# Optimization experiments

Hardware: AMD Instinct MI355X
Metric: run time of the kernel (lower is better)

Reference implementation:

```python
import jax, jax.numpy as jnp
import numpy as np

B, D = 4096, 768

def setup_inputs() -> dict:
    key = jax.random.key(0)
    k1, k2 = jax.random.split(key)
    embeddings = jax.random.normal(k1, (B, D), dtype=jnp.float32)
    # precomputed articulatory distance matrix (stand-in for articulatory_distance_fn over word pairs)
    art_dist = jax.random.uniform(k2, (B, B), dtype=jnp.float32)
    return {"embeddings": embeddings, "art_dist": art_dist}

def reference(embeddings, art_dist):
    b = embeddings.shape[0]
    # pairwise squared L2 distances via Gram matrix: ||ei||^2 + ||ej||^2 - 2 ei.ej
    sq = jnp.sum(embeddings * embeddings, axis=1)                  # [B]
    gram = jnp.einsum('id,jd->ij', embeddings, embeddings)         # [B, B]
    d2 = sq[:, None] + sq[None, :] - 2.0 * gram                    # [B, B]
    off_diag = 1.0 - jnp.eye(b, dtype=embeddings.dtype)            # exclude i == j
    pair_loss = (d2 - art_dist) ** 2
    pairs_count = b * (b - 1)
    return jnp.sum(pair_loss * off_diag) / pairs_count
```

## Files before the change

### kernel.cpp

```cpp
#include <hip/hip_runtime.h>
#include <hip/hip_bf16.h>

#define B_DIM 4096
#define D_DIM 768
#define BM 128
#define BN 128
#define BK 64

typedef __bf16 bf16_t;
typedef bf16_t bf16x8 __attribute__((ext_vector_type(8)));
typedef float f32x4 __attribute__((ext_vector_type(4)));

__global__ __launch_bounds__(256) void prep_kernel(
    const float* __restrict__ E, ushort* __restrict__ Ebf, float* __restrict__ sq)
{
    const int row = blockIdx.x;
    const int tid = threadIdx.x;
    const float* er = E + (size_t)row * D_DIM;
    ushort* br = Ebf + (size_t)row * D_DIM;
    float s = 0.f;
    #pragma unroll
    for (int c = tid; c < D_DIM; c += 256) {
        float v = er[c];
        s += v * v;
        __hip_bfloat16 h = __float2bfloat16(v);
        br[c] = *reinterpret_cast<const ushort*>(&h);
    }
    #pragma unroll
    for (int off = 32; off > 0; off >>= 1) s += __shfl_down(s, off);
    __shared__ float red[4];
    if ((tid & 63) == 0) red[tid >> 6] = s;
    __syncthreads();
    if (tid == 0) sq[row] = red[0] + red[1] + red[2] + red[3];
}

__global__ __launch_bounds__(256) void gram_loss_kernel(
    const ushort* __restrict__ Ebf, const float* __restrict__ sq,
    const float* __restrict__ art, float* __restrict__ out)
{
    __shared__ ushort Als[BM][BK];
    __shared__ ushort Bls[BN][BK];
    __shared__ float red[4];

    const int tid  = threadIdx.x;
    const int lane = tid & 63;
    const int wave = tid >> 6;
    const int wr = wave >> 1;
    const int wc = wave & 1;
    const int tileR = blockIdx.x >> 5;
    const int tileC = blockIdx.x & 31;
    const int row0 = tileR * BM;
    const int col0 = tileC * BN;

    f32x4 acc[4][4] = {};

    const int srow  = tid >> 3;
    const int scol8 = (tid & 7) * 8;

    for (int kk = 0; kk < D_DIM; kk += BK) {
        #pragma unroll
        for (int i = 0; i < 4; ++i) {
            const int r = i * 32 + srow;
            const int colg = scol8 ^ ((r & 7) << 3);
            const ushort* gA = Ebf + (size_t)(row0 + r) * D_DIM + kk + colg;
            __builtin_amdgcn_global_load_lds(
                (const __attribute__((address_space(1))) void*)gA,
                (__attribute__((address_space(3))) void*)(&Als[r][scol8]),
                16, 0, 0);
            const ushort* gB = Ebf + (size_t)(col0 + r) * D_DIM + kk + colg;
            __builtin_amdgcn_global_load_lds(
                (const __attribute__((address_space(1))) void*)gB,
                (__attribute__((address_space(3))) void*)(&Bls[r][scol8]),
                16, 0, 0);
        }
        __syncthreads();

        #pragma unroll
        for (int k2 = 0; k2 < BK; k2 += 32) {
            bf16x8 af[4], bfr[4];
            #pragma unroll
            for (int m = 0; m < 4; ++m) {
                const int r = wr * 64 + m * 16 + (lane & 15);
                const int c = (k2 + (lane >> 4) * 8) ^ ((r & 7) << 3);
                af[m] = *reinterpret_cast<const bf16x8*>(&Als[r][c]);
            }
            #pragma unroll
            for (int n = 0; n < 4; ++n) {
                const int r = wc * 64 + n * 16 + (lane & 15);
                const int c = (k2 + (lane >> 4) * 8) ^ ((r & 7) << 3);
                bfr[n] = *reinterpret_cast<const bf16x8*>(&Bls[r][c]);
            }
            #pragma unroll
            for (int m = 0; m < 4; ++m)
                #pragma unroll
                for (int n = 0; n < 4; ++n)
                    acc[m][n] = __builtin_amdgcn_mfma_f32_16x16x32_bf16(
                        af[m], bfr[n], acc[m][n], 0, 0, 0);
        }
        __syncthreads();
    }

    float lsum = 0.f;
    const int lr = (lane >> 4) * 4;
    const int lc = lane & 15;
    const int rbase = row0 + wr * 64;
    const int cbase = col0 + wc * 64;
    #pragma unroll
    for (int m = 0; m < 4; ++m) {
        const int gi0 = rbase + m * 16 + lr;
        #pragma unroll
        for (int n = 0; n < 4; ++n) {
            const int gj = cbase + n * 16 + lc;
            const float sqj = sq[gj];
            #pragma unroll
            for (int j = 0; j < 4; ++j) {
                const int gi = gi0 + j;
                const float d2 = sq[gi] + sqj - 2.0f * acc[m][n][j];
                const float t = d2 - art[(size_t)gi * B_DIM + gj];
                if (gi != gj) lsum += t * t;
            }
        }
    }
    #pragma unroll
    for (int off = 32; off > 0; off >>= 1) lsum += __shfl_down(lsum, off);
    if (lane == 0) red[wave] = lsum;
    __syncthreads();
    if (tid == 0) {
        const float inv_pairs = 1.0f / ((float)B_DIM * (float)(B_DIM - 1));
        atomicAdd(out, (red[0] + red[1] + red[2] + red[3]) * inv_pairs);
    }
}

extern "C" void kernel_launch(void* const* d_in, const int* in_sizes, int n_in,
                              void* d_out, int out_size, void* d_ws, size_t ws_size,
                              hipStream_t stream) {
    const float* E   = (const float*)d_in[0];
    const float* art = (const float*)d_in[1];
    float* out = (float*)d_out;

    ushort* Ebf = (ushort*)d_ws;
    float*  sq  = (float*)((char*)d_ws + (size_t)B_DIM * D_DIM * 2);

    hipMemsetAsync(d_out, 0, sizeof(float), stream);
    prep_kernel<<<B_DIM, 256, 0, stream>>>(E, Ebf, sq);
    gram_loss_kernel<<<(B_DIM / BM) * (B_DIM / BN), 256, 0, stream>>>(Ebf, sq, art, out);
}
```

Measured before the change: 145.3 us.

## Exploit Gram symmetry: compute upper-triangular tiles, read both art halves

Because the Gram matrix is symmetric, the main kernel now launches only upper-triangular tile pairs (528 instead of 1024). Each off-diagonal tile scores both art[i][j] and art[j][i] against the same d2, which roughly halves the MFMA work while still reading all of art. The transposed art read is vectorised as float4 along columns. The prep kernel also changes to one wave per row with float4 loads and no shared-memory reduction. The cost is an uneven tile-index decode loop and transposed art loads that may coalesce less well.

```diff
diff --git a/kernel.cpp b/kernel.cpp
--- a/kernel.cpp
+++ b/kernel.cpp
@@ -6,32 +6,36 @@
 #define BM 128
 #define BN 128
 #define BK 64
+#define NT (B_DIM / BM)
 
 typedef __bf16 bf16_t;
 typedef bf16_t bf16x8 __attribute__((ext_vector_type(8)));
 typedef float f32x4 __attribute__((ext_vector_type(4)));
 
+static __device__ __forceinline__ ushort f2bf(float v) {
+    __hip_bfloat16 h = __float2bfloat16(v);
+    return *reinterpret_cast<const ushort*>(&h);
+}
+
 __global__ __launch_bounds__(256) void prep_kernel(
     const float* __restrict__ E, ushort* __restrict__ Ebf, float* __restrict__ sq)
 {
-    const int row = blockIdx.x;
-    const int tid = threadIdx.x;
-    const float* er = E + (size_t)row * D_DIM;
-    ushort* br = Ebf + (size_t)row * D_DIM;
+    const int lane = threadIdx.x & 63;
+    const int row  = blockIdx.x * 4 + (threadIdx.x >> 6);
+    const float4* er = reinterpret_cast<const float4*>(E + (size_t)row * D_DIM);
+    ushort4* br = reinterpret_cast<ushort4*>(Ebf + (size_t)row * D_DIM);
     float s = 0.f;
     #pragma unroll
-    for (int c = tid; c < D_DIM; c += 256) {
-        float v = er[c];
-        s += v * v;
-        __hip_bfloat16 h = __float2bfloat16(v);
-        br[c] = *reinterpret_cast<const ushort*>(&h);
+    for (int k = 0; k < 3; ++k) {
+        float4 v = er[lane + 64 * k];
+        s += v.x * v.x + v.y * v.y + v.z * v.z + v.w * v.w;
+        ushort4 o;
+        o.x = f2bf(v.x); o.y = f2bf(v.y); o.z = f2bf(v.z); o.w = f2bf(v.w);
+        br[lane + 64 * k] = o;
     }
     #pragma unroll
     for (int off = 32; off > 0; off >>= 1) s += __shfl_down(s, off);
-    __shared__ float red[4];
-    if ((tid & 63) == 0) red[tid >> 6] = s;
-    __syncthreads();
-    if (tid == 0) sq[row] = red[0] + red[1] + red[2] + red[3];
+    if (lane == 0) sq[row] = s;
 }
 
 __global__ __launch_bounds__(256) void gram_loss_kernel(
@@ -47,10 +51,12 @@
     const int wave = tid >> 6;
     const int wr = wave >> 1;
     const int wc = wave & 1;
-    const int tileR = blockIdx.x >> 5;
-    const int tileC = blockIdx.x & 31;
-    const int row0 = tileR * BM;
-    const int col0 = tileC * BN;
+
+    int b = blockIdx.x, I = 0, rem = NT;
+    while (b >= rem) { b -= rem; ++I; --rem; }
+    const int J = I + b;
+    const int row0 = I * BM;
+    const int col0 = J * BN;
 
     f32x4 acc[4][4] = {};
 
@@ -105,22 +111,47 @@
     const int lc = lane & 15;
     const int rbase = row0 + wr * 64;
     const int cbase = col0 + wc * 64;
-    #pragma unroll
-    for (int m = 0; m < 4; ++m) {
-        const int gi0 = rbase + m * 16 + lr;
+
+    if (I != J) {
         #pragma unroll
-        for (int n = 0; n < 4; ++n) {
-            const int gj = cbase + n * 16 + lc;
-            const float sqj = sq[gj];
+        for (int m = 0; m < 4; ++m) {
+            const int gi0 = rbase + m * 16 + lr;
             #pragma unroll
-            for (int j = 0; j < 4; ++j) {
-                const int gi = gi0 + j;
-                const float d2 = sq[gi] + sqj - 2.0f * acc[m][n][j];
-                const float t = d2 - art[(size_t)gi * B_DIM + gj];
-                if (gi != gj) lsum += t * t;
+            for (int n = 0; n < 4; ++n) {
+                const int gj = cbase + n * 16 + lc;
+                const float sqj = sq[gj];
+                const float4 am = *reinterpret_cast<const float4*>(
+                    &art[(size_t)gj * B_DIM + gi0]);
+                const float amv[4] = { am.x, am.y, am.z, am.w };
+                #pragma unroll
+                for (int j = 0; j < 4; ++j) {
+                    const int gi = gi0 + j;
+                    const float d2 = sq[gi] + sqj - 2.0f * acc[m][n][j];
+                    const float t1 = d2 - art[(size_t)gi * B_DIM + gj];
+                    const float t2 = d2 - amv[j];
+                    lsum += t1 * t1 + t2 * t2;
+                }
+            }
+        }
+    } else {
+        #pragma unroll
+        for (int m = 0; m < 4; ++m) {
+            const int gi0 = rbase + m * 16 + lr;
+            #pragma unroll
+            for (int n = 0; n < 4; ++n) {
+                const int gj = cbase + n * 16 + lc;
+                const float sqj = sq[gj];
+                #pragma unroll
+                for (int j = 0; j < 4; ++j) {
+                    const int gi = gi0 + j;
+                    const float d2 = sq[gi] + sqj - 2.0f * acc[m][n][j];
+                    const float t = d2 - art[(size_t)gi * B_DIM + gj];
+                    if (gi != gj) lsum += t * t;
+                }
             }
         }
     }
+
     #pragma unroll
     for (int off = 32; off > 0; off >>= 1) lsum += __shfl_down(lsum, off);
     if (lane == 0) red[wave] = lsum;
@@ -142,6 +173,6 @@
     float*  sq  = (float*)((char*)d_ws + (size_t)B_DIM * D_DIM * 2);
 
     hipMemsetAsync(d_out, 0, sizeof(float), stream);
-    prep_kernel<<<B_DIM, 256, 0, stream>>>(E, Ebf, sq);
-    gram_loss_kernel<<<(B_DIM / BM) * (B_DIM / BN), 256, 0, stream>>>(Ebf, sq, art, out);
+    prep_kernel<<<B_DIM / 4, 256, 0, stream>>>(E, Ebf, sq);
+    gram_loss_kernel<<<(NT * (NT + 1)) / 2, 256, 0, stream>>>(Ebf, sq, art, out);
 }
```

Result: slower. 151.3 us (+4.1%).
